# Kernel tuning notes

Hardware: AMD Instinct MI355X
Metric: run time of the kernel (lower is better)

The kernel has to match this reference:

```python
import jax, jax.numpy as jnp
import numpy as np

K = 5          # up_kernel
G = 1          # up_group
S = 2          # scale_factor


def conv2d(x, w, b, pad):
    y = jax.lax.conv_general_dilated(
        x, w, window_strides=(1, 1), padding=[(pad, pad), (pad, pad)],
        dimension_numbers=('NCHW', 'OIHW', 'NCHW'))
    return y + b[None, :, None, None]


def pixel_shuffle(x, r):
    n, c, h, w = x.shape
    x = x.reshape(n, c // (r * r), r, r, h, w)
    x = x.transpose(0, 1, 4, 2, 5, 3)  # n, c', h, r, w, r
    return x.reshape(n, c // (r * r), h * r, w * r)


def setup_inputs() -> dict:
    key = jax.random.key(0)
    k1, k2, k3 = jax.random.split(key, 3)
    x = jax.random.normal(k1, (8, 256, 64, 64), dtype=jnp.float32)
    w_comp = jax.random.normal(k2, (64, 256, 1, 1), dtype=jnp.float32) * 0.05
    b_comp = jnp.zeros((64,), dtype=jnp.float32)
    w_enc = jax.random.normal(k3, (100, 64, 3, 3), dtype=jnp.float32) * 0.001
    b_enc = jnp.zeros((100,), dtype=jnp.float32)
    return {"x": x, "w_comp": w_comp, "b_comp": b_comp, "w_enc": w_enc, "b_enc": b_enc}


def reference(x, w_comp, b_comp, w_enc, b_enc):
    n, c, h, w = x.shape
    kk = K * K
    # channel compressor (1x1) + content encoder (3x3, pad 1)
    comp = conv2d(x, w_comp, b_comp, pad=0)
    mask = conv2d(comp, w_enc, b_enc, pad=1)          # (n, kk*G*S*S, h, w)
    # kernel normalizer: pixel_shuffle then softmax over the kk taps
    mask = pixel_shuffle(mask, S)                      # (n, kk*G, H, W)
    H, W = h * S, w * S
    mask = mask.reshape(n, G, kk, H, W)
    mask = jax.nn.softmax(mask, axis=2)
    # CARAFE reassembly: each output pixel gathers KxK neighborhood of its
    # low-res source pixel (i//S, j//S) with the learned normalized weights.
    r = (K - 1) // 2
    xp = jnp.pad(x, ((0, 0), (0, 0), (r, r), (r, r)))
    cg = c // G
    out = jnp.zeros((n, c, H, W), dtype=x.dtype)
    for idx in range(kk):  # small fixed loop over kernel taps (25)
        dy, dx = idx // K, idx % K
        patch = xp[:, :, dy:dy + h, dx:dx + w]                     # (n,c,h,w)
        patch_up = jnp.repeat(jnp.repeat(patch, S, axis=2), S, axis=3)  # (n,c,H,W)
        wgt = mask[:, :, idx]                                      # (n,G,H,W)
        out = out + (patch_up.reshape(n, G, cg, H, W) * wgt[:, :, None]).reshape(n, c, H, W)
    return out
```

## Files before the change

kernel.cpp:

```cpp
#include <hip/hip_runtime.h>


#define CI 256

typedef __attribute__((ext_vector_type(8))) short bf16x8;
typedef __attribute__((ext_vector_type(4))) float f32x4;
typedef __attribute__((ext_vector_type(2))) float f32x2;

__device__ inline unsigned short f2bf(float f) {
    unsigned u = __float_as_uint(f);
    unsigned r = (u + 0x7FFF + ((u >> 16) & 1)) >> 16;
    return (unsigned short)r;
}

__device__ inline unsigned cvt_pk_bf16(float lo, float hi) {
    unsigned r;
    asm("v_cvt_pk_bf16_f32 %0, %1, %2" : "=v"(r) : "v"(lo), "v"(hi));
    return r;
}

__device__ inline float bf_lo(unsigned u) { return __int_as_float(u << 16); }
__device__ inline float bf_hi(unsigned u) { return __int_as_float(u & 0xffff0000u); }

__device__ inline void pk_fma_lo(f32x2& acc, f32x2 m, f32x2 s) {
    asm("v_pk_fma_f32 %0, %1, %2, %0 op_sel_hi:[1,0,1]" : "+v"(acc) : "v"(m), "v"(s));
}
__device__ inline void pk_fma_hi(f32x2& acc, f32x2 m, f32x2 s) {
    asm("v_pk_fma_f32 %0, %1, %2, %0 op_sel:[0,1,0] op_sel_hi:[1,1,1]" : "+v"(acc) : "v"(m), "v"(s));
}

__device__ inline void nt_store2(float* p, f32x2 v) {
    __builtin_nontemporal_store(__builtin_bit_cast(unsigned long long, v),
                                (unsigned long long*)p);
}

__global__ __launch_bounds__(256) void prep_small(const float* __restrict__ w_comp,
                                                  unsigned short* __restrict__ wA,
                                                  float* __restrict__ zp) {
    int i = blockIdx.x * 256 + threadIdx.x;
    if (i < 64) zp[i] = 0.f;
    if (i < 64 * 256) wA[i] = f2bf(w_comp[i]);
}

__global__ __launch_bounds__(64) void conv1x1_mfma(const float* __restrict__ x,
                                                   const unsigned short* __restrict__ wA,
                                                   const float* __restrict__ b_comp,
                                                   const float* __restrict__ w_enc,
                                                   unsigned short* __restrict__ comp,
                                                   unsigned short* __restrict__ Bp) {
    int l = threadIdx.x;
    int b = blockIdx.x;

    if (b >= 1024) {
        int idx = (b - 1024) * 64 + l;
        int j = idx & 7;
        int n = (idx >> 3) % 112;
        int g = idx / (112 * 8);
        int k = g * 8 + j;
        int tap = k >> 6;
        int c = k & 63;
        float v = (n < 100) ? w_enc[n * 576 + c * 9 + tap] : 0.f;
        Bp[idx] = f2bf(v);
        return;
    }

    int c16 = l & 15;
    int lq  = l >> 4;
    int bs  = (b & 7) * 128 + (b >> 3);
    int P0  = bs * 32;
    int nimg = P0 >> 12;
    int hw   = P0 & 4095;

    const float* xp = x + (size_t)nimg * CI * 4096 + hw + c16;

    f32x4 acc[4][2];
#pragma unroll
    for (int mt = 0; mt < 4; mt++)
#pragma unroll
        for (int pt = 0; pt < 2; pt++) acc[mt][pt] = f32x4{0.f, 0.f, 0.f, 0.f};

#pragma unroll
    for (int ks = 0; ks < 8; ks++) {
        int k0 = ks * 32 + lq * 8;
        float v0[8], v1[8];
#pragma unroll
        for (int j = 0; j < 8; j++) {
            const float* pj = xp + (size_t)(k0 + j) * 4096;
            v0[j] = pj[0];
            v1[j] = pj[16];
        }
        bf16x8 xb0, xb1;
#pragma unroll
        for (int j = 0; j < 8; j++) {
            xb0[j] = (short)f2bf(v0[j]);
            xb1[j] = (short)f2bf(v1[j]);
        }
#pragma unroll
        for (int mt = 0; mt < 4; mt++) {
            bf16x8 wf = *(const bf16x8*)(wA + (mt * 16 + c16) * 256 + k0);
            acc[mt][0] = __builtin_amdgcn_mfma_f32_16x16x32_bf16(wf, xb0, acc[mt][0], 0, 0, 0);
            acc[mt][1] = __builtin_amdgcn_mfma_f32_16x16x32_bf16(wf, xb1, acc[mt][1], 0, 0, 0);
        }
    }

#pragma unroll
    for (int pt = 0; pt < 2; pt++) {
        unsigned short* cp = comp + (size_t)(P0 + pt * 16 + c16) * 64;
#pragma unroll
        for (int mt = 0; mt < 4; mt++) {
            int och0 = mt * 16 + lq * 4;
            float4 bb = *reinterpret_cast<const float4*>(b_comp + och0);
            unsigned u0 = f2bf(acc[mt][pt][0] + bb.x) | (f2bf(acc[mt][pt][1] + bb.y) << 16);
            unsigned u1 = f2bf(acc[mt][pt][2] + bb.z) | (f2bf(acc[mt][pt][3] + bb.w) << 16);
            reinterpret_cast<uint2*>(cp + och0)[0] = uint2{u0, u1};
        }
    }
}

__global__ __launch_bounds__(256) void conv3x3_mfma(const unsigned short* __restrict__ comp,
                                                    const unsigned short* __restrict__ Bp,
                                                    const float* __restrict__ b_enc,
                                                    const float* __restrict__ zp,
                                                    unsigned* __restrict__ maskP) {
    __shared__ char Bs[2][5 * 7168];
    int tid = threadIdx.x;
    int wv  = tid >> 6;
    int l   = tid & 63;
    int c16 = l & 15;
    int lq  = l >> 4;
    int b   = blockIdx.x;
    int bs  = (b & 7) * 64 + (b >> 3);
    int nimg = bs >> 6;
    int h    = bs & 63;
    int w0   = wv * 16;

    const char* cbase = (const char*)(comp + (size_t)nimg * 4096 * 64);
    const char* zpb   = (const char*)zp;
    const char* Bpb   = (const char*)Bp;

#define STAGEPH(s0_, cnt_, buf_)                                                          \
    {                                                                                     \
        const char* src_ = Bpb + (s0_)*7168 + l * 16;                                     \
        for (int inst_ = wv; inst_ < 7 * (cnt_); inst_ += 4) {                            \
            __builtin_amdgcn_global_load_lds(                                             \
                (const __attribute__((address_space(1))) void*)(src_ + inst_ * 1024),     \
                (__attribute__((address_space(3))) void*)(&Bs[buf_][inst_ * 1024]),       \
                16, 0, 0);                                                                \
        }                                                                                 \
    }

    f32x4 acc[7];
#pragma unroll
    for (int nt = 0; nt < 7; nt++) acc[nt] = f32x4{0.f, 0.f, 0.f, 0.f};

    const int dyt[9] = {-1, -1, -1, 0, 0, 0, 1, 1, 1};
    const int dxt[9] = {-1, 0, 1, -1, 0, 1, -1, 0, 1};

    STAGEPH(0, 5, 0);
    __syncthreads();

#pragma unroll
    for (int ph = 0; ph < 4; ph++) {
        int s0  = ph * 5;
        int cnt = (s0 + 5 <= 18) ? 5 : (18 - s0);
        int cur = ph & 1;
        if (ph < 3) {
            int ns0  = s0 + 5;
            int ncnt = (ns0 + 5 <= 18) ? 5 : (18 - ns0);
            STAGEPH(ns0, ncnt, cur ^ 1);
        }
        for (int ss = 0; ss < cnt; ss++) {
            int s = s0 + ss;
            int tap = s >> 1, half = s & 1;
            int hh = h + dyt[tap];
            int ww = w0 + c16 + dxt[tap];
            const char* ap = ((unsigned)hh < 64u && (unsigned)ww < 64u)
                                 ? cbase + (hh * 64 + ww) * 128 : zpb;
            bf16x8 a = *(const bf16x8*)(ap + lq * 16 + half * 64);

            bf16x8 bf[7];
#pragma unroll
            for (int nt = 0; nt < 7; nt++)
                bf[nt] = *(const bf16x8*)(&Bs[cur][ss * 7168 + (lq * 112 + nt * 16 + c16) * 16]);
#pragma unroll
            for (int nt = 0; nt < 7; nt++)
                acc[nt] = __builtin_amdgcn_mfma_f32_16x16x32_bf16(a, bf[nt], acc[nt], 0, 0, 0);
        }
        __syncthreads();
    }
#undef STAGEPH

    float bias[7];
#pragma unroll
    for (int nt = 0; nt < 7; nt++) {
        int n = nt * 16 + c16;
        bias[nt] = (n < 100) ? b_enc[n] : 0.f;
    }
    int nvalid = (c16 < 4) ? 7 : 6;

    unsigned* mbase = maskP + ((size_t)nimg * 64 + h) * 3200;

#pragma unroll
    for (int r = 0; r < 4; r++) {
        float v[7];
#pragma unroll
        for (int nt = 0; nt < 7; nt++) v[nt] = acc[nt][r] + bias[nt];
        float m = v[0];
#pragma unroll
        for (int nt = 1; nt < 7; nt++) if (nt < nvalid) m = fmaxf(m, v[nt]);
        m = fmaxf(m, __shfl_xor(m, 4));
        m = fmaxf(m, __shfl_xor(m, 8));
        float e[7];
        float s = 0.f;
#pragma unroll
        for (int nt = 0; nt < 7; nt++) {
            e[nt] = (nt < nvalid) ? __expf(v[nt] - m) : 0.f;
            s += e[nt];
        }
        s += __shfl_xor(s, 4);
        s += __shfl_xor(s, 8);
        float inv = 1.f / s;
        int wpix = w0 + lq * 4 + r;
#pragma unroll
        for (int nt = 0; nt < 7; nt++) {
            float mine = (nt < nvalid) ? e[nt] * inv : 0.f;
            float part = __shfl_xor(mine, 1);
            if (((c16 & 1) == 0) && (nt * 16 + c16) < 100) {
                unsigned pk = cvt_pk_bf16(mine, part);
                mbase[(nt * 8 + (c16 >> 1)) * 64 + wpix] = pk;
            }
        }
    }
}

__global__ __launch_bounds__(256) void reassemble(const float* __restrict__ x,
                                                  const unsigned* __restrict__ maskP,
                                                  float* __restrict__ out) {
    int lane = threadIdx.x & 63;
    int cq   = threadIdx.x >> 6;
    int b    = blockIdx.x;
    int bs   = (b & 7) * 256 + (b >> 3);
    int cgb  = bs & 3;
    int h    = (bs >> 2) & 63;
    int n    = bs >> 8;
    int c0   = cgb * 64 + cq * 16;

    const unsigned* mrow = maskP + ((size_t)n * 64 + h) * 3200 + lane;

    int   yy[5];
    float vmy[5], vmx[5];
#pragma unroll
    for (int d = 0; d < 5; d++) {
        int y  = h + d - 2;
        int xc = lane + d - 2;
        yy[d]  = min(max(y, 0), 63) * 64;
        vmy[d] = ((unsigned)y  < 64u) ? 1.f : 0.f;
        vmx[d] = ((unsigned)xc < 64u) ? 1.f : 0.f;
    }

    f32x2 msk2[50];
#pragma unroll
    for (int t = 0; t < 25; t++) {
        float f = vmy[t / 5] * vmx[t % 5];
        unsigned u0 = mrow[(2 * t + 0) * 64];
        unsigned u1 = mrow[(2 * t + 1) * 64];
        f32x2 m01, m23;
        m01.x = bf_lo(u0); m01.y = bf_hi(u0);
        m23.x = bf_lo(u1); m23.y = bf_hi(u1);
        msk2[2 * t + 0] = m01 * f;
        msk2[2 * t + 1] = m23 * f;
    }

    int idxm2 = ((lane - 2) & 63) << 2;
    int idxm1 = ((lane - 1) & 63) << 2;
    int idxp1 = ((lane + 1) & 63) << 2;
    int idxp2 = ((lane + 2) & 63) << 2;

    const float* xbase = x + ((size_t)(n * CI + c0)) * 4096 + lane;
    float*       obase = out + ((size_t)(n * CI + c0) * 128 + 2 * h) * 128 + 2 * lane;

    float ra[5], rb[5];
    unsigned pk[5];
#pragma unroll
    for (int d = 0; d < 5; d++) {
        ra[d] = xbase[yy[d]];
        rb[d] = xbase[4096 + yy[d]];
        pk[d] = cvt_pk_bf16(ra[d], rb[d]);
    }

    for (int p = 0; p < 8; p++) {
        const float* xn = xbase + (size_t)((p < 7) ? (2 * p + 2) : 0) * 4096;
        float na[5], nb[5];
#pragma unroll
        for (int d = 0; d < 5; d++) {
            na[d] = xn[yy[d]];
            nb[d] = xn[4096 + yy[d]];
        }

        f32x2 A0 = {0.f, 0.f}, A1 = {0.f, 0.f};
        f32x2 B0 = {0.f, 0.f}, B1 = {0.f, 0.f};
#pragma unroll
        for (int d = 0; d < 5; d++) {
            int pv = (int)pk[d];
            int sm2 = __builtin_amdgcn_ds_bpermute(idxm2, pv);
            int sm1 = __builtin_amdgcn_ds_bpermute(idxm1, pv);
            int sp1 = __builtin_amdgcn_ds_bpermute(idxp1, pv);
            int sp2 = __builtin_amdgcn_ds_bpermute(idxp2, pv);
            f32x2 s[5];
            s[0].x = bf_lo((unsigned)sm2); s[0].y = bf_hi((unsigned)sm2);
            s[1].x = bf_lo((unsigned)sm1); s[1].y = bf_hi((unsigned)sm1);
            s[2].x = ra[d];                s[2].y = rb[d];
            s[3].x = bf_lo((unsigned)sp1); s[3].y = bf_hi((unsigned)sp1);
            s[4].x = bf_lo((unsigned)sp2); s[4].y = bf_hi((unsigned)sp2);
            const f32x2* mk2 = msk2 + d * 10;
#pragma unroll
            for (int k = 0; k < 5; k++) {
                pk_fma_lo(A0, mk2[2 * k + 0], s[k]);
                pk_fma_lo(A1, mk2[2 * k + 1], s[k]);
                pk_fma_hi(B0, mk2[2 * k + 0], s[k]);
                pk_fma_hi(B1, mk2[2 * k + 1], s[k]);
            }
        }
        float* opa = obase + (size_t)(2 * p) * 16384;
        float* opb = opa + 16384;
        nt_store2(opa, A0);
        nt_store2(opa + 128, A1);
        nt_store2(opb, B0);
        nt_store2(opb + 128, B1);

#pragma unroll
        for (int d = 0; d < 5; d++) {
            ra[d] = na[d];
            rb[d] = nb[d];
            pk[d] = cvt_pk_bf16(na[d], nb[d]);
        }
    }
}

extern "C" void kernel_launch(void* const* d_in, const int* in_sizes, int n_in,
                              void* d_out, int out_size, void* d_ws, size_t ws_size,
                              hipStream_t stream) {
    const float* x      = (const float*)d_in[0];
    const float* w_comp = (const float*)d_in[1];
    const float* b_comp = (const float*)d_in[2];
    const float* w_enc  = (const float*)d_in[3];
    const float* b_enc  = (const float*)d_in[4];
    float* out = (float*)d_out;

    char* ws = (char*)d_ws;
    float*          zp    = (float*)(ws + 0);
    unsigned short* wA    = (unsigned short*)(ws + 256);
    unsigned short* Bp    = (unsigned short*)(ws + 33024);
    unsigned short* comp  = (unsigned short*)(ws + 162048);
    unsigned*       maskP = (unsigned*)(ws + 4356352);

    prep_small<<<64, 256, 0, stream>>>(w_comp, wA, zp);
    conv1x1_mfma<<<1024 + 1008, 64, 0, stream>>>(x, wA, b_comp, w_enc, comp, Bp);
    conv3x3_mfma<<<512, 256, 0, stream>>>(comp, Bp, b_enc, zp, maskP);
    reassemble<<<2048, 256, 0, stream>>>(x, maskP, out);
}
```

Baseline: 65.87 us.

## Fuse 3x3 conv softmax with CARAFE reassembly through LDS mask

Merges the content-encoder conv/softmax kernel and the reassembly kernel into one. The normalized mask row is kept in shared memory, padded to a stride of 65 to avoid bank conflicts, instead of going through a global buffer. Each block now reassembles all 256 channels for its row (64 channels per wave), and the weight staging changes to 6 phases of 3 slices to reduce LDS use. This removes the mask round trip to global memory and one launch. In exchange the grid drops from 2048 to 512 blocks for the memory-heavy reassembly, so each wave runs a longer serial loop and latency hiding may suffer.

```diff
diff --git a/kernel.cpp b/kernel.cpp
--- a/kernel.cpp
+++ b/kernel.cpp
@@ -117,12 +117,15 @@
     }
 }
 
-__global__ __launch_bounds__(256) void conv3x3_mfma(const unsigned short* __restrict__ comp,
-                                                    const unsigned short* __restrict__ Bp,
-                                                    const float* __restrict__ b_enc,
-                                                    const float* __restrict__ zp,
-                                                    unsigned* __restrict__ maskP) {
-    __shared__ char Bs[2][5 * 7168];
+__global__ __launch_bounds__(256) void conv3x3_reasm(const unsigned short* __restrict__ comp,
+                                                     const unsigned short* __restrict__ Bp,
+                                                     const float* __restrict__ b_enc,
+                                                     const float* __restrict__ zp,
+                                                     const float* __restrict__ x,
+                                                     float* __restrict__ out) {
+    __shared__ char Bs[2][3 * 7168];
+    __shared__ unsigned mask_lds[3250];
+
     int tid = threadIdx.x;
     int wv  = tid >> 6;
     int l   = tid & 63;
@@ -138,10 +141,10 @@
     const char* zpb   = (const char*)zp;
     const char* Bpb   = (const char*)Bp;
 
-#define STAGEPH(s0_, cnt_, buf_)                                                          \
+#define STAGEPH(s0_, buf_)                                                                \
     {                                                                                     \
         const char* src_ = Bpb + (s0_)*7168 + l * 16;                                     \
-        for (int inst_ = wv; inst_ < 7 * (cnt_); inst_ += 4) {                            \
+        for (int inst_ = wv; inst_ < 21; inst_ += 4) {                                    \
             __builtin_amdgcn_global_load_lds(                                             \
                 (const __attribute__((address_space(1))) void*)(src_ + inst_ * 1024),     \
                 (__attribute__((address_space(3))) void*)(&Bs[buf_][inst_ * 1024]),       \
@@ -156,20 +159,15 @@
     const int dyt[9] = {-1, -1, -1, 0, 0, 0, 1, 1, 1};
     const int dxt[9] = {-1, 0, 1, -1, 0, 1, -1, 0, 1};
 
-    STAGEPH(0, 5, 0);
+    STAGEPH(0, 0);
     __syncthreads();
 
 #pragma unroll
-    for (int ph = 0; ph < 4; ph++) {
-        int s0  = ph * 5;
-        int cnt = (s0 + 5 <= 18) ? 5 : (18 - s0);
+    for (int ph = 0; ph < 6; ph++) {
+        int s0  = ph * 3;
         int cur = ph & 1;
-        if (ph < 3) {
-            int ns0  = s0 + 5;
-            int ncnt = (ns0 + 5 <= 18) ? 5 : (18 - ns0);
-            STAGEPH(ns0, ncnt, cur ^ 1);
-        }
-        for (int ss = 0; ss < cnt; ss++) {
+        if (ph < 5) STAGEPH(s0 + 3, cur ^ 1);
+        for (int ss = 0; ss < 3; ss++) {
             int s = s0 + ss;
             int tap = s >> 1, half = s & 1;
             int hh = h + dyt[tap];
@@ -190,69 +188,58 @@
     }
 #undef STAGEPH
 
-    float bias[7];
-#pragma unroll
-    for (int nt = 0; nt < 7; nt++) {
-        int n = nt * 16 + c16;
-        bias[nt] = (n < 100) ? b_enc[n] : 0.f;
-    }
-    int nvalid = (c16 < 4) ? 7 : 6;
-
-    unsigned* mbase = maskP + ((size_t)nimg * 64 + h) * 3200;
-
-#pragma unroll
-    for (int r = 0; r < 4; r++) {
-        float v[7];
-#pragma unroll
-        for (int nt = 0; nt < 7; nt++) v[nt] = acc[nt][r] + bias[nt];
-        float m = v[0];
-#pragma unroll
-        for (int nt = 1; nt < 7; nt++) if (nt < nvalid) m = fmaxf(m, v[nt]);
-        m = fmaxf(m, __shfl_xor(m, 4));
-        m = fmaxf(m, __shfl_xor(m, 8));
-        float e[7];
-        float s = 0.f;
+    {
+        float bias[7];
 #pragma unroll
         for (int nt = 0; nt < 7; nt++) {
-            e[nt] = (nt < nvalid) ? __expf(v[nt] - m) : 0.f;
-            s += e[nt];
-        }
-        s += __shfl_xor(s, 4);
-        s += __shfl_xor(s, 8);
-        float inv = 1.f / s;
-        int wpix = w0 + lq * 4 + r;
-#pragma unroll
-        for (int nt = 0; nt < 7; nt++) {
-            float mine = (nt < nvalid) ? e[nt] * inv : 0.f;
-            float part = __shfl_xor(mine, 1);
-            if (((c16 & 1) == 0) && (nt * 16 + c16) < 100) {
-                unsigned pk = cvt_pk_bf16(mine, part);
-                mbase[(nt * 8 + (c16 >> 1)) * 64 + wpix] = pk;
+            int n = nt * 16 + c16;
+            bias[nt] = (n < 100) ? b_enc[n] : 0.f;
+        }
+        int nvalid = (c16 < 4) ? 7 : 6;
+
+#pragma unroll
+        for (int r = 0; r < 4; r++) {
+            float v[7];
+#pragma unroll
+            for (int nt = 0; nt < 7; nt++) v[nt] = acc[nt][r] + bias[nt];
+            float m = v[0];
+#pragma unroll
+            for (int nt = 1; nt < 7; nt++) if (nt < nvalid) m = fmaxf(m, v[nt]);
+            m = fmaxf(m, __shfl_xor(m, 4));
+            m = fmaxf(m, __shfl_xor(m, 8));
+            float e[7];
+            float s = 0.f;
+#pragma unroll
+            for (int nt = 0; nt < 7; nt++) {
+                e[nt] = (nt < nvalid) ? __expf(v[nt] - m) : 0.f;
+                s += e[nt];
             }
-        }
-    }
-}
-
-__global__ __launch_bounds__(256) void reassemble(const float* __restrict__ x,
-                                                  const unsigned* __restrict__ maskP,
-                                                  float* __restrict__ out) {
-    int lane = threadIdx.x & 63;
-    int cq   = threadIdx.x >> 6;
-    int b    = blockIdx.x;
-    int bs   = (b & 7) * 256 + (b >> 3);
-    int cgb  = bs & 3;
-    int h    = (bs >> 2) & 63;
-    int n    = bs >> 8;
-    int c0   = cgb * 64 + cq * 16;
-
-    const unsigned* mrow = maskP + ((size_t)n * 64 + h) * 3200 + lane;
+            s += __shfl_xor(s, 4);
+            s += __shfl_xor(s, 8);
+            float inv = 1.f / s;
+            int wpix = w0 + lq * 4 + r;
+#pragma unroll
+            for (int nt = 0; nt < 7; nt++) {
+                float mine = (nt < nvalid) ? e[nt] * inv : 0.f;
+                float part = __shfl_xor(mine, 1);
+                if (((c16 & 1) == 0) && (nt * 16 + c16) < 100) {
+                    unsigned pk = cvt_pk_bf16(mine, part);
+                    mask_lds[(nt * 8 + (c16 >> 1)) * 65 + wpix] = pk;
+                }
+            }
+        }
+    }
+    __syncthreads();
+
+    int c0 = wv * 64;
+    const unsigned* mrow = mask_lds + l;
 
     int   yy[5];
     float vmy[5], vmx[5];
 #pragma unroll
     for (int d = 0; d < 5; d++) {
         int y  = h + d - 2;
-        int xc = lane + d - 2;
+        int xc = l + d - 2;
         yy[d]  = min(max(y, 0), 63) * 64;
         vmy[d] = ((unsigned)y  < 64u) ? 1.f : 0.f;
         vmx[d] = ((unsigned)xc < 64u) ? 1.f : 0.f;
@@ -262,8 +249,8 @@
 #pragma unroll
     for (int t = 0; t < 25; t++) {
         float f = vmy[t / 5] * vmx[t % 5];
-        unsigned u0 = mrow[(2 * t + 0) * 64];
-        unsigned u1 = mrow[(2 * t + 1) * 64];
+        unsigned u0 = mrow[(2 * t + 0) * 65];
+        unsigned u1 = mrow[(2 * t + 1) * 65];
         f32x2 m01, m23;
         m01.x = bf_lo(u0); m01.y = bf_hi(u0);
         m23.x = bf_lo(u1); m23.y = bf_hi(u1);
@@ -271,13 +258,13 @@
         msk2[2 * t + 1] = m23 * f;
     }
 
-    int idxm2 = ((lane - 2) & 63) << 2;
-    int idxm1 = ((lane - 1) & 63) << 2;
-    int idxp1 = ((lane + 1) & 63) << 2;
-    int idxp2 = ((lane + 2) & 63) << 2;
-
-    const float* xbase = x + ((size_t)(n * CI + c0)) * 4096 + lane;
-    float*       obase = out + ((size_t)(n * CI + c0) * 128 + 2 * h) * 128 + 2 * lane;
+    int idxm2 = ((l - 2) & 63) << 2;
+    int idxm1 = ((l - 1) & 63) << 2;
+    int idxp1 = ((l + 1) & 63) << 2;
+    int idxp2 = ((l + 2) & 63) << 2;
+
+    const float* xbase = x + ((size_t)(nimg * CI + c0)) * 4096 + l;
+    float*       obase = out + ((size_t)(nimg * CI + c0) * 128 + 2 * h) * 128 + 2 * l;
 
     float ra[5], rb[5];
     unsigned pk[5];
@@ -288,8 +275,8 @@
         pk[d] = cvt_pk_bf16(ra[d], rb[d]);
     }
 
-    for (int p = 0; p < 8; p++) {
-        const float* xn = xbase + (size_t)((p < 7) ? (2 * p + 2) : 0) * 4096;
+    for (int p = 0; p < 32; p++) {
+        const float* xn = xbase + (size_t)((p < 31) ? (2 * p + 2) : 0) * 4096;
         float na[5], nb[5];
 #pragma unroll
         for (int d = 0; d < 5; d++) {
@@ -348,14 +335,12 @@
     float* out = (float*)d_out;
 
     char* ws = (char*)d_ws;
-    float*          zp    = (float*)(ws + 0);
-    unsigned short* wA    = (unsigned short*)(ws + 256);
-    unsigned short* Bp    = (unsigned short*)(ws + 33024);
-    unsigned short* comp  = (unsigned short*)(ws + 162048);
-    unsigned*       maskP = (unsigned*)(ws + 4356352);
+    float*          zp   = (float*)(ws + 0);
+    unsigned short* wA   = (unsigned short*)(ws + 256);
+    unsigned short* Bp   = (unsigned short*)(ws + 33024);
+    unsigned short* comp = (unsigned short*)(ws + 162048);
 
     prep_small<<<64, 256, 0, stream>>>(w_comp, wA, zp);
     conv1x1_mfma<<<1024 + 1008, 64, 0, stream>>>(x, wA, b_comp, w_enc, comp, Bp);
-    conv3x3_mfma<<<512, 256, 0, stream>>>(comp, Bp, b_enc, zp, maskP);
-    reassemble<<<2048, 256, 0, stream>>>(x, maskP, out);
-}
+    conv3x3_reasm<<<512, 256, 0, stream>>>(comp, Bp, b_enc, zp, x, out);
+}
```

Result: faster. 60.98 us (-7.4%).
